# Kernel optimization log

Measured on AMD Instinct MI355X. Metric: run time of the kernel, lower is better.

Reference implementation:

```python
import jax, jax.numpy as jnp
import numpy as np

B, D, L, K = 4096, 1024, 16384, 64


def setup_inputs() -> dict:
    key = jax.random.key(0)
    k1, k2, k3, k4, k5 = jax.random.split(key, 5)
    x = jax.random.normal(k1, (B, D), dtype=jnp.float32)
    # torch nn.Linear weights are [out_features, in_features]
    W_enc = jax.random.normal(k2, (L, D), dtype=jnp.float32) * (1.0 / np.sqrt(D))
    b_enc = jax.random.normal(k3, (L,), dtype=jnp.float32) * 0.01
    W_dec = jax.random.normal(k4, (D, L), dtype=jnp.float32) * (1.0 / np.sqrt(L))
    b_dec = jax.random.normal(k5, (D,), dtype=jnp.float32) * 0.01
    return {"x": x, "W_enc": W_enc, "b_enc": b_enc, "W_dec": W_dec, "b_dec": b_dec}


def reference(x, W_enc, b_enc, W_dec, b_dec):
    # xbar = x - decoder.bias
    xbar = x - b_dec                                   # [B, D]
    a = jnp.einsum('bd,ld->bl', xbar, W_enc) + b_enc   # [B, L]
    vals, idx = jax.lax.top_k(a, K)                    # [B, K]
    f = jnp.zeros_like(a)
    rows = jnp.arange(a.shape[0])[:, None]             # [B, 1]
    f = f.at[rows, idx].set(jax.nn.relu(vals))         # sparse latent [B, L]
    xhat = jnp.einsum('bl,dl->bd', f, W_dec) + b_dec   # [B, D]
    return (f, xhat)
```

## Files before the change

### kernel.cpp

```cpp
#include <hip/hip_runtime.h>

#define B_N 4096
#define D_N 1024
#define L_N 16384
#define K_N 64
#define CAP 512
#define CNT_STRIDE 16

typedef __attribute__((ext_vector_type(8))) short bf16x8;
typedef __attribute__((ext_vector_type(4))) float f32x4;

__device__ __forceinline__ unsigned short f2bf(float f) {
  union { float f; unsigned int u; } v; v.f = f;
  unsigned int r = v.u + 0x7FFFu + ((v.u >> 16) & 1u);
  return (unsigned short)(r >> 16);
}
__device__ __forceinline__ float bf2f(unsigned short u) {
  union { unsigned int u; float f; } v; v.u = (unsigned int)u << 16;
  return v.f;
}

__global__ __launch_bounds__(256) void prep_all(const float* __restrict__ x,
                                                const float* __restrict__ W_enc,
                                                const float* __restrict__ W_dec,
                                                const float* __restrict__ b_dec,
                                                unsigned short* __restrict__ wencb,
                                                unsigned short* __restrict__ xbarb,
                                                float* __restrict__ srow,
                                                unsigned short* __restrict__ WdTb,
                                                int* __restrict__ cand_cnt) {
  __shared__ float tile[32][33];
  __shared__ float wsum[4];
  const int t = threadIdx.x;
  const int bid = blockIdx.x;
  if (bid < 16384) {
    size_t i = (size_t)bid * 256 + t;
    float4 v = ((const float4*)W_enc)[i];
    ushort4 o;
    o.x = f2bf(v.x); o.y = f2bf(v.y); o.z = f2bf(v.z); o.w = f2bf(v.w);
    ((ushort4*)wencb)[i] = o;
  } else if (bid < 20480) {
    const int b = bid - 16384;
    if (t == 0) cand_cnt[b * CNT_STRIDE] = 0;
    float4 v = ((const float4*)x)[(size_t)b * 256 + t];
    float4 bd = ((const float4*)b_dec)[t];
    float4 e = make_float4(v.x - bd.x, v.y - bd.y, v.z - bd.z, v.w - bd.w);
    ushort4 o;
    o.x = f2bf(e.x); o.y = f2bf(e.y); o.z = f2bf(e.z); o.w = f2bf(e.w);
    ((ushort4*)xbarb)[(size_t)b * 256 + t] = o;
    float ss = e.x * e.x + e.y * e.y + e.z * e.z + e.w * e.w;
#pragma unroll
    for (int off = 32; off; off >>= 1) ss += __shfl_down(ss, off);
    if ((t & 63) == 0) wsum[t >> 6] = ss;
    __syncthreads();
    if (t == 0) srow[b] = sqrtf((wsum[0] + wsum[1] + wsum[2] + wsum[3]) * (1.0f / D_N));
  } else {
    const int tb = bid - 20480;
    const int l0 = (tb & 511) * 32;
    const int d0 = (tb >> 9) * 32;
    const int tx = t & 31, ty = t >> 5;
    for (int i = ty; i < 32; i += 8)
      tile[i][tx] = W_dec[(size_t)(d0 + i) * L_N + l0 + tx];
    __syncthreads();
    for (int i = ty; i < 32; i += 8)
      WdTb[(size_t)(l0 + i) * D_N + d0 + tx] = f2bf(tile[tx][i]);
  }
}

__global__ __launch_bounds__(256) void gemm_enc_select(
    const unsigned short* __restrict__ A,
    const unsigned short* __restrict__ Bw,
    const float* __restrict__ b_enc,
    const float* __restrict__ srow,
    int* __restrict__ cand_cnt,
    float* __restrict__ cand_val,
    int* __restrict__ cand_idx,
    float* __restrict__ f) {
  __shared__ __align__(16) unsigned short lA[128 * 32];
  __shared__ __align__(16) unsigned short lB[128 * 32];
  __shared__ float thrLDS[128];
  __shared__ float beLDS[128];
  const int tid = threadIdx.x;
  const int wave = tid >> 6, lane = tid & 63;
  const int bm = blockIdx.x, bn = blockIdx.y;
  const int m0 = (wave & 1) * 64, n0 = (wave >> 1) * 64;
  const int fr = lane & 15, quad = lane >> 4;

  if (tid < 128) {
    thrLDS[tid] = 2.3f * srow[bm * 128 + tid];
    beLDS[tid] = b_enc[bn * 128 + tid];
  }

  f32x4 acc[4][4];
#pragma unroll
  for (int i = 0; i < 4; ++i)
#pragma unroll
    for (int j = 0; j < 4; ++j) acc[i][j] = (f32x4){0.f, 0.f, 0.f, 0.f};

  const int rA = lane >> 2;
  const int cA = (lane & 3) * 8;
  const size_t baseA = (size_t)(bm * 128) * D_N;
  const size_t baseB = (size_t)(bn * 128) * D_N;

  for (int k0 = 0; k0 < D_N; k0 += 32) {
    __syncthreads();
#pragma unroll
    for (int i = 0; i < 2; ++i) {
      const int rb = (wave * 2 + i) * 16;
      const unsigned short* gA = A + baseA + (size_t)(rb + rA) * D_N + k0 + cA;
      const unsigned short* gB = Bw + baseB + (size_t)(rb + rA) * D_N + k0 + cA;
      __builtin_amdgcn_global_load_lds((const __attribute__((address_space(1))) void*)gA,
                                       (__attribute__((address_space(3))) void*)&lA[rb * 32],
                                       16, 0, 0);
      __builtin_amdgcn_global_load_lds((const __attribute__((address_space(1))) void*)gB,
                                       (__attribute__((address_space(3))) void*)&lB[rb * 32],
                                       16, 0, 0);
    }
    __syncthreads();

    bf16x8 af[4], bfr[4];
#pragma unroll
    for (int i = 0; i < 4; ++i)
      af[i] = *(const bf16x8*)&lA[(m0 + i * 16 + fr) * 32 + quad * 8];
#pragma unroll
    for (int j = 0; j < 4; ++j)
      bfr[j] = *(const bf16x8*)&lB[(n0 + j * 16 + fr) * 32 + quad * 8];
#pragma unroll
    for (int i = 0; i < 4; ++i)
#pragma unroll
      for (int j = 0; j < 4; ++j)
        acc[i][j] = __builtin_amdgcn_mfma_f32_16x16x32_bf16(af[i], bfr[j], acc[i][j], 0, 0, 0);
  }

  const int lrow0 = m0 + quad * 4;
  const int lcol0 = n0 + fr;
#pragma unroll
  for (int i = 0; i < 4; ++i) {
#pragma unroll
    for (int j = 0; j < 4; ++j) {
      const int lcol = lcol0 + j * 16;
      const float be = beLDS[lcol];
#pragma unroll
      for (int r = 0; r < 4; ++r) {
        const int lrow = lrow0 + i * 16 + r;
        const float val = acc[i][j][r] + be;
        if (val > thrLDS[lrow]) {
          const int grow = bm * 128 + lrow;
          const int p = atomicAdd(&cand_cnt[grow * CNT_STRIDE], 1);
          if (p < CAP) {
            cand_val[(size_t)grow * CAP + p] = val;
            cand_idx[(size_t)grow * CAP + p] = bn * 128 + lcol;
          }
        }
      }
    }
  }

  {
    const float4 z4 = make_float4(0.f, 0.f, 0.f, 0.f);
    float4* fz = (float4*)(f + (size_t)(bm * 128) * L_N + bn * 128);
#pragma unroll
    for (int it = 0; it < 16; ++it) {
      const int idx = it * 256 + tid;
      const int r = idx >> 5, c = idx & 31;
      fz[(size_t)r * (L_N / 4) + c] = z4;
    }
  }
}

__global__ __launch_bounds__(256) void select_decode(
    const float* __restrict__ x,
    const float* __restrict__ W_enc,
    const float* __restrict__ b_enc,
    const float* __restrict__ b_dec,
    const float* __restrict__ srow,
    const int* __restrict__ cand_cnt,
    const float* __restrict__ cand_val,
    const int* __restrict__ cand_idx,
    const unsigned short* __restrict__ WdTb,
    float* __restrict__ f,
    float* __restrict__ xhat) {
  const int b = blockIdx.x, t = threadIdx.x;
  const int lane = t & 63, wave = t >> 6;
  __shared__ double xd[D_N];
  __shared__ float cv[CAP];
  __shared__ int ci[CAP];
  __shared__ double bu[128];
  __shared__ int bidx[128];
  __shared__ int o_idx[K_N];
  __shared__ float o_val[K_N];
  __shared__ int sidx[K_N];
  __shared__ float sval[K_N];
  __shared__ int nb_s, nin_s, outcnt;
  __shared__ float v64_s;

  const int cnt = min(cand_cnt[b * CNT_STRIDE], CAP);
  if (t == 0) { nb_s = 0; nin_s = 0; outcnt = 0; v64_s = -1e30f; }
  for (int c = t; c < cnt; c += 256) {
    cv[c] = cand_val[(size_t)b * CAP + c];
    ci[c] = cand_idx[(size_t)b * CAP + c];
  }
  for (int i = t; i < D_N; i += 256)
    xd[i] = (double)x[(size_t)b * D_N + i] - (double)b_dec[i];
  __syncthreads();

  for (int c = t; c < cnt; c += 256) {
    const float v = cv[c];
    const int id = ci[c];
    int r = 0;
    for (int k = 0; k < cnt; ++k)
      r += (cv[k] > v || (cv[k] == v && ci[k] < id)) ? 1 : 0;
    if (r == 63) v64_s = v;
  }
  __syncthreads();
  const float v64 = v64_s;
  const float m = 0.04f * srow[b];

  for (int c = t; c < cnt; c += 256) {
    const float v = cv[c];
    if (v > v64 + m) {
      atomicAdd(&nin_s, 1);
    } else if (v >= v64 - m) {
      const int p = atomicAdd(&nb_s, 1);
      if (p < 128) bidx[p] = c;
    }
  }
  __syncthreads();
  const int nb = min(nb_s, 128);
  const int nin = nin_s;
  int nneed = K_N - nin;
  if (nneed < 0) nneed = 0;

  for (int c = wave; c < nb; c += 4) {
    const int l = ci[bidx[c]];
    const float4* wr = (const float4*)(W_enc + (size_t)l * D_N);
    double acc = 0.0;
#pragma unroll
    for (int j = 0; j < 4; ++j) {
      float4 w4 = wr[j * 64 + lane];
      const int base = (j * 64 + lane) * 4;
      acc += xd[base + 0] * (double)w4.x + xd[base + 1] * (double)w4.y +
             xd[base + 2] * (double)w4.z + xd[base + 3] * (double)w4.w;
    }
#pragma unroll
    for (int off = 32; off; off >>= 1) acc += __shfl_down(acc, off);
    if (lane == 0) bu[c] = acc + (double)b_enc[l];
  }
  __syncthreads();

  for (int c = t; c < cnt; c += 256) {
    if (cv[c] > v64 + m) {
      const int p = atomicAdd(&outcnt, 1);
      if (p < K_N) { o_idx[p] = ci[c]; o_val[p] = cv[c]; }
    }
  }
  if (t < nb) {
    const double uv = bu[t];
    const int l = ci[bidx[t]];
    int r = 0;
    for (int k = 0; k < nb; ++k)
      r += (bu[k] > uv || (bu[k] == uv && ci[bidx[k]] < l)) ? 1 : 0;
    if (r < nneed) {
      const int p = atomicAdd(&outcnt, 1);
      if (p < K_N) { o_idx[p] = l; o_val[p] = (float)uv; }
    }
  }
  __syncthreads();
  const int ns = min(outcnt, K_N);

  if (t < K_N) {
    sidx[t] = (t < ns) ? o_idx[t] : t;
    sval[t] = (t < ns) ? fmaxf(o_val[t], 0.0f) : 0.0f;
  }
  __syncthreads();

  if (t < ns) f[(size_t)b * L_N + sidx[t]] = sval[t];

  float4 acc = ((const float4*)b_dec)[t];
#pragma unroll 8
  for (int k = 0; k < K_N; ++k) {
    const float v = sval[k];
    const ushort4 w = ((const ushort4*)(WdTb + (size_t)sidx[k] * D_N))[t];
    acc.x += v * bf2f(w.x); acc.y += v * bf2f(w.y);
    acc.z += v * bf2f(w.z); acc.w += v * bf2f(w.w);
  }
  ((float4*)(xhat + (size_t)b * D_N))[t] = acc;
}

extern "C" void kernel_launch(void* const* d_in, const int* in_sizes, int n_in,
                              void* d_out, int out_size, void* d_ws, size_t ws_size,
                              hipStream_t stream) {
  (void)in_sizes; (void)n_in; (void)out_size; (void)ws_size;
  const float* x     = (const float*)d_in[0];
  const float* W_enc = (const float*)d_in[1];
  const float* b_enc = (const float*)d_in[2];
  const float* W_dec = (const float*)d_in[3];
  const float* b_dec = (const float*)d_in[4];

  float* f    = (float*)d_out;
  float* xhat = (float*)d_out + (size_t)B_N * L_N;

  char* ws = (char*)d_ws;
  unsigned short* wencb = (unsigned short*)ws;
  unsigned short* xbarb = (unsigned short*)(ws + 33554432);
  unsigned short* WdTb  = (unsigned short*)(ws + 41943040);
  float* srow           = (float*)(ws + 75497472);
  int* cand_cnt         = (int*)(ws + 75513856);
  float* cand_val       = (float*)(ws + 75776000);
  int* cand_idx         = (int*)(ws + 84164608);

  prep_all<<<36864, 256, 0, stream>>>(x, W_enc, W_dec, b_dec, wencb, xbarb, srow,
                                      WdTb, cand_cnt);
  gemm_enc_select<<<dim3(B_N / 128, L_N / 128), 256, 0, stream>>>(
      xbarb, wencb, b_enc, srow, cand_cnt, cand_val, cand_idx, f);
  select_decode<<<B_N, 256, 0, stream>>>(x, W_enc, b_enc, b_dec, srow,
                                         cand_cnt, cand_val, cand_idx, WdTb, f, xhat);
}
```

Before: 797.7 us.

## Rewrite encoder GEMM with 256x256 tiles, double-buffered swizzled LDS and XCD-aware block mapping

The encoder GEMM moves from 128x128 tiles with 256 threads and a K-step of 32 to 256x256 tiles with 512 threads, a K-step of 64, and double-buffered 128KB LDS staging. The next tile is prefetched while MFMAs run, and an XOR swizzle on LDS columns avoids bank conflicts. Blocks are remapped so that consecutive blocks on the same XCD share tiles, and wave priority is raised around the MFMA bursts. The aim is more data reuse per byte loaded and latency hiding, at the cost of heavy LDS use (one block per CU) and more accumulator registers.

```diff
diff --git a/kernel.cpp b/kernel.cpp
--- a/kernel.cpp
+++ b/kernel.cpp
@@ -67,7 +67,7 @@
   }
 }
 
-__global__ __launch_bounds__(256) void gemm_enc_select(
+__global__ __launch_bounds__(512, 2) void gemm_enc_select(
     const unsigned short* __restrict__ A,
     const unsigned short* __restrict__ Bw,
     const float* __restrict__ b_enc,
@@ -76,80 +76,100 @@
     float* __restrict__ cand_val,
     int* __restrict__ cand_idx,
     float* __restrict__ f) {
-  __shared__ __align__(16) unsigned short lA[128 * 32];
-  __shared__ __align__(16) unsigned short lB[128 * 32];
-  __shared__ float thrLDS[128];
-  __shared__ float beLDS[128];
+  __shared__ __align__(16) char smem[131072];
   const int tid = threadIdx.x;
-  const int wave = tid >> 6, lane = tid & 63;
-  const int bm = blockIdx.x, bn = blockIdx.y;
-  const int m0 = (wave & 1) * 64, n0 = (wave >> 1) * 64;
+  const int wid = tid >> 6, lane = tid & 63;
+  const int wm = wid >> 2, wn = wid & 3;
   const int fr = lane & 15, quad = lane >> 4;
 
-  if (tid < 128) {
-    thrLDS[tid] = 2.3f * srow[bm * 128 + tid];
-    beLDS[tid] = b_enc[bn * 128 + tid];
-  }
-
-  f32x4 acc[4][4];
-#pragma unroll
-  for (int i = 0; i < 4; ++i)
+  const int wg = ((blockIdx.x & 7) << 7) + (blockIdx.x >> 3);
+  const int bm = wg & 15, bn = wg >> 4;
+
+  const int stgrow = wid * 8 + (lane >> 3);
+  const int scol = ((lane & 7) ^ (lane >> 3)) << 4;
+  const char* gA = (const char*)A + ((size_t)(bm * 256 + stgrow) * D_N) * 2 + scol;
+  const char* gB = (const char*)Bw + ((size_t)(bn * 256 + stgrow) * D_N) * 2 + scol;
+
+#define STAGE(kt_, p_)                                                                   \
+  {                                                                                      \
+    const size_t ko_ = (size_t)(kt_)*128;                                                \
+    _Pragma("unroll") for (int r_ = 0; r_ < 4; ++r_) {                                   \
+      __builtin_amdgcn_global_load_lds(                                                  \
+          (const __attribute__((address_space(1))) void*)(gA + (size_t)r_ * 131072 + ko_), \
+          (__attribute__((address_space(3))) void*)(smem + (p_)*65536 + r_ * 8192 + wid * 1024), \
+          16, 0, 0);                                                                     \
+      __builtin_amdgcn_global_load_lds(                                                  \
+          (const __attribute__((address_space(1))) void*)(gB + (size_t)r_ * 131072 + ko_), \
+          (__attribute__((address_space(3))) void*)(smem + (p_)*65536 + 32768 + r_ * 8192 + wid * 1024), \
+          16, 0, 0);                                                                     \
+    }                                                                                    \
+  }
+
+  f32x4 acc[8][4];
+#pragma unroll
+  for (int i = 0; i < 8; ++i)
 #pragma unroll
     for (int j = 0; j < 4; ++j) acc[i][j] = (f32x4){0.f, 0.f, 0.f, 0.f};
 
-  const int rA = lane >> 2;
-  const int cA = (lane & 3) * 8;
-  const size_t baseA = (size_t)(bm * 128) * D_N;
-  const size_t baseB = (size_t)(bn * 128) * D_N;
-
-  for (int k0 = 0; k0 < D_N; k0 += 32) {
-    __syncthreads();
-#pragma unroll
-    for (int i = 0; i < 2; ++i) {
-      const int rb = (wave * 2 + i) * 16;
-      const unsigned short* gA = A + baseA + (size_t)(rb + rA) * D_N + k0 + cA;
-      const unsigned short* gB = Bw + baseB + (size_t)(rb + rA) * D_N + k0 + cA;
-      __builtin_amdgcn_global_load_lds((const __attribute__((address_space(1))) void*)gA,
-                                       (__attribute__((address_space(3))) void*)&lA[rb * 32],
-                                       16, 0, 0);
-      __builtin_amdgcn_global_load_lds((const __attribute__((address_space(1))) void*)gB,
-                                       (__attribute__((address_space(3))) void*)&lB[rb * 32],
-                                       16, 0, 0);
-    }
-    __syncthreads();
-
-    bf16x8 af[4], bfr[4];
-#pragma unroll
-    for (int i = 0; i < 4; ++i)
-      af[i] = *(const bf16x8*)&lA[(m0 + i * 16 + fr) * 32 + quad * 8];
-#pragma unroll
-    for (int j = 0; j < 4; ++j)
-      bfr[j] = *(const bf16x8*)&lB[(n0 + j * 16 + fr) * 32 + quad * 8];
-#pragma unroll
-    for (int i = 0; i < 4; ++i)
-#pragma unroll
-      for (int j = 0; j < 4; ++j)
-        acc[i][j] = __builtin_amdgcn_mfma_f32_16x16x32_bf16(af[i], bfr[j], acc[i][j], 0, 0, 0);
-  }
-
-  const int lrow0 = m0 + quad * 4;
-  const int lcol0 = n0 + fr;
-#pragma unroll
-  for (int i = 0; i < 4; ++i) {
-#pragma unroll
-    for (int j = 0; j < 4; ++j) {
-      const int lcol = lcol0 + j * 16;
-      const float be = beLDS[lcol];
-#pragma unroll
-      for (int r = 0; r < 4; ++r) {
-        const int lrow = lrow0 + i * 16 + r;
-        const float val = acc[i][j][r] + be;
-        if (val > thrLDS[lrow]) {
-          const int grow = bm * 128 + lrow;
+  const int aB = (wm * 128 + fr) * 128;
+  const int bB = 32768 + (wn * 64 + fr) * 128;
+  const int s0 = (quad ^ (fr & 7)) << 4;
+
+  STAGE(0, 0);
+  __syncthreads();
+
+#define PHASE(mh_, ks_, TRAIL_)                                                          \
+  {                                                                                      \
+    bf16x8 af[4], bv[4];                                                                 \
+    _Pragma("unroll") for (int i_ = 0; i_ < 4; ++i_)                                     \
+        af[i_] = *(const bf16x8*)(smem + pb + aB + ((mh_)*64 + i_ * 16) * 128 +          \
+                                  (s0 ^ ((ks_)*64)));                                    \
+    _Pragma("unroll") for (int j_ = 0; j_ < 4; ++j_)                                     \
+        bv[j_] = *(const bf16x8*)(smem + pb + bB + j_ * 2048 + (s0 ^ ((ks_)*64)));       \
+    __builtin_amdgcn_s_barrier();                                                        \
+    asm volatile("s_waitcnt lgkmcnt(0)" ::: "memory");                                   \
+    __builtin_amdgcn_sched_barrier(0);                                                   \
+    __builtin_amdgcn_s_setprio(1);                                                       \
+    _Pragma("unroll") for (int i_ = 0; i_ < 4; ++i_)                                     \
+        _Pragma("unroll") for (int j_ = 0; j_ < 4; ++j_)                                 \
+            acc[(mh_)*4 + i_][j_] = __builtin_amdgcn_mfma_f32_16x16x32_bf16(             \
+                af[i_], bv[j_], acc[(mh_)*4 + i_][j_], 0, 0, 0);                         \
+    __builtin_amdgcn_s_setprio(0);                                                       \
+    if (TRAIL_) __builtin_amdgcn_s_barrier();                                            \
+  }
+
+  for (int kt = 0; kt < D_N / 64; ++kt) {
+    const int pb = (kt & 1) * 65536;
+    if (kt < D_N / 64 - 1) STAGE(kt + 1, (kt & 1) ^ 1);
+    PHASE(0, 0, 1)
+    PHASE(1, 0, 1)
+    PHASE(0, 1, 1)
+    PHASE(1, 1, 0)
+    if (kt < D_N / 64 - 1) {
+      asm volatile("s_waitcnt vmcnt(0)" ::: "memory");
+      __builtin_amdgcn_s_barrier();
+    }
+  }
+
+  const int lc0 = bn * 256 + wn * 64 + fr;
+  float be[4];
+#pragma unroll
+  for (int nj = 0; nj < 4; ++nj) be[nj] = b_enc[lc0 + nj * 16];
+  const int gr0 = bm * 256 + wm * 128 + quad * 4;
+#pragma unroll
+  for (int mi = 0; mi < 8; ++mi) {
+#pragma unroll
+    for (int r = 0; r < 4; ++r) {
+      const int grow = gr0 + mi * 16 + r;
+      const float thr = 2.3f * srow[grow];
+#pragma unroll
+      for (int nj = 0; nj < 4; ++nj) {
+        const float val = acc[mi][nj][r] + be[nj];
+        if (val > thr) {
           const int p = atomicAdd(&cand_cnt[grow * CNT_STRIDE], 1);
           if (p < CAP) {
             cand_val[(size_t)grow * CAP + p] = val;
-            cand_idx[(size_t)grow * CAP + p] = bn * 128 + lcol;
+            cand_idx[(size_t)grow * CAP + p] = lc0 + nj * 16;
           }
         }
       }
@@ -158,14 +178,16 @@
 
   {
     const float4 z4 = make_float4(0.f, 0.f, 0.f, 0.f);
-    float4* fz = (float4*)(f + (size_t)(bm * 128) * L_N + bn * 128);
-#pragma unroll
-    for (int it = 0; it < 16; ++it) {
-      const int idx = it * 256 + tid;
-      const int r = idx >> 5, c = idx & 31;
-      fz[(size_t)r * (L_N / 4) + c] = z4;
-    }
-  }
+    float4* fz = (float4*)(f + (size_t)(bm * 256) * L_N + bn * 256);
+#pragma unroll
+    for (int it = 0; it < 32; ++it) {
+      const int idx = it * 512 + tid;
+      const int rr = idx >> 6, cc = idx & 63;
+      fz[(size_t)rr * (L_N / 4) + cc] = z4;
+    }
+  }
+#undef STAGE
+#undef PHASE
 }
 
 __global__ __launch_bounds__(256) void select_decode(
@@ -311,7 +333,7 @@
 
   prep_all<<<36864, 256, 0, stream>>>(x, W_enc, W_dec, b_dec, wencb, xbarb, srow,
                                       WdTb, cand_cnt);
-  gemm_enc_select<<<dim3(B_N / 128, L_N / 128), 256, 0, stream>>>(
+  gemm_enc_select<<<1024, 512, 0, stream>>>(
       xbarb, wencb, b_enc, srow, cand_cnt, cand_val, cand_idx, f);
   select_decode<<<B_N, 256, 0, stream>>>(x, W_enc, b_enc, b_dec, srow,
                                          cand_cnt, cand_val, cand_idx, WdTb, f, xhat);
```

Measured after the change: 833.3 us. 1.04x slower.
